# Kernel optimization log

Measured on AMD Instinct MI355X. Metric: run time of the kernel, lower is better.

The kernel has to match this reference:

```python
import jax, jax.numpy as jnp
import numpy as np

B, TQ, TK, N = 4, 128, 512, 1024   # batch, query len, key len, key_size
QS, VS, OS = 1024, 1024, 1024      # query_size, value_size, output_size


def setup_inputs() -> dict:
    key = jax.random.key(0)
    ks = jax.random.split(key, 9)
    s_q = 1.0 / np.sqrt(QS)
    s_k = 1.0 / np.sqrt(N)
    s_o = 1.0 / np.sqrt(QS + VS)
    return {
        "query": jax.random.normal(ks[0], (B, TQ, QS), jnp.float32),
        "keys": jax.random.normal(ks[1], (B, TK, N), jnp.float32),
        "values": jax.random.normal(ks[2], (B, TK, VS), jnp.float32),
        # linear_q: query_size -> key_size
        "Wq": jax.random.normal(ks[3], (N, QS), jnp.float32) * s_q,
        "bq": jax.random.normal(ks[4], (N,), jnp.float32) * s_q,
        # linear_att: key_size -> 1
        "w_att": jax.random.normal(ks[5], (N,), jnp.float32) * s_k,
        "b_att": jax.random.normal(ks[6], (), jnp.float32) * s_k,
        # linear_out: (query_size + value_size) -> output_size
        "Wout": jax.random.normal(ks[7], (OS, QS + VS), jnp.float32) * s_o,
        "bout": jax.random.normal(ks[8], (OS,), jnp.float32) * s_o,
    }


def reference(query, keys, values, Wq, bq, w_att, b_att, Wout, bout):
    # linear_q: [b, t_q, query_size] -> [b, t_q, n]
    att_query = jnp.einsum("bqe,ne->bqn", query, Wq) + bq
    # Bahdanau additive score: tanh(q + k) then linear_att (n -> 1)
    # intermediate is [b, t_q, t_k, n] as in the original module
    sum_qk = jnp.tanh(att_query[:, :, None, :] + keys[:, None, :, :])
    scores = jnp.einsum("bqkn,n->bqk", sum_qk, w_att) + b_att  # [b, t_q, t_k]
    scores_normalized = jax.nn.softmax(scores, axis=2)
    # context = softmax(scores) @ values  (dropout is identity with p=0)
    context = jnp.einsum("bqk,bkv->bqv", scores_normalized, values)
    # linear_out on concat([query, context]) + tanh
    cat = jnp.concatenate([query, context], axis=2)  # [b, t_q, q+v]
    out = jnp.tanh(jnp.einsum("bqc,oc->bqo", cat, Wout) + bout)
    return out, scores_normalized
```

## Files before the change

kernel.cpp:

```cpp
#include <hip/hip_runtime.h>
#include <math.h>

static constexpr int B_  = 4;
static constexpr int TQ  = 128;
static constexpr int TK  = 512;
static constexpr int NN  = 1024;
static constexpr int QS  = 1024;
static constexpr int VS  = 1024;
static constexpr int OS  = 1024;

#define K2F    2.8853900817779268f
#define LOG2EF 1.4426950408889634f
#define SLICE  524288

typedef __attribute__((ext_vector_type(8))) short bf16x8;
typedef __attribute__((ext_vector_type(4))) float f32x4;

#define MFMA16(a,b,c) __builtin_amdgcn_mfma_f32_16x16x32_bf16((a),(b),(c),0,0,0)

__device__ __forceinline__ ushort bf16_rne(float x) {
    uint u = __float_as_uint(x);
    u += 0x7FFFu + ((u >> 16) & 1u);
    return (ushort)(u >> 16);
}
__device__ __forceinline__ void split2(float x, ushort& h, ushort& l) {
    ushort hh = bf16_rne(x);
    float hv = __uint_as_float((uint)hh << 16);
    h = hh;
    l = bf16_rne(x - hv);
}

__global__ __launch_bounds__(256) void cvt_all_kernel(
    const float* __restrict__ Q, const float* __restrict__ Wq,
    const float* __restrict__ Wo, const float* __restrict__ V,
    ushort* __restrict__ Qh, ushort* __restrict__ Ql,
    ushort* __restrict__ Wqh, ushort* __restrict__ Wql,
    ushort* __restrict__ Woh,
    ushort* __restrict__ Vth)
{
    __shared__ float tile[64][65];
    const int bid = blockIdx.x;
    const int t = threadIdx.x;
    if (bid < 3584) {
        if (bid < 1536) {
            const float* src; ushort *h, *l; int idx;
            if (bid < 512) { src = Q;  h = Qh;  l = Ql;  idx = bid*256 + t; }
            else           { src = Wq; h = Wqh; l = Wql; idx = (bid-512)*256 + t; }
            float4 v = ((const float4*)src)[idx];
            ushort4 hh, ll;
            split2(v.x, hh.x, ll.x); split2(v.y, hh.y, ll.y);
            split2(v.z, hh.z, ll.z); split2(v.w, hh.w, ll.w);
            ((ushort4*)h)[idx] = hh;
            ((ushort4*)l)[idx] = ll;
        } else {
            int idx = (bid-1536)*256 + t;
            float4 v = ((const float4*)Wo)[idx];
            ushort4 hh;
            hh.x = bf16_rne(v.x); hh.y = bf16_rne(v.y);
            hh.z = bf16_rne(v.z); hh.w = bf16_rne(v.w);
            ((ushort4*)Woh)[idx] = hh;
        }
        return;
    }
    const int vid = bid - 3584;
    const int v0 = (vid & 15) * 64;
    const int k0 = ((vid >> 4) & 7) * 64;
    const int b  = vid >> 7;
    const float* src = V + ((size_t)b*TK + k0)*VS + v0;
    #pragma unroll
    for (int p = 0; p < 4; ++p) {
        int r = (t >> 4) + p*16, c = (t & 15) * 4;
        float4 vv = *(const float4*)(src + (size_t)r*VS + c);
        tile[r][c] = vv.x; tile[r][c+1] = vv.y; tile[r][c+2] = vv.z; tile[r][c+3] = vv.w;
    }
    __syncthreads();
    ushort* dh = Vth + (size_t)b*(VS*TK) + (size_t)v0*TK + k0;
    #pragma unroll
    for (int p = 0; p < 4; ++p) {
        int vr = (t >> 4) + p*16, kc = (t & 15) * 4;
        ushort4 hh;
        hh.x = bf16_rne(tile[kc+0][vr]);
        hh.y = bf16_rne(tile[kc+1][vr]);
        hh.z = bf16_rne(tile[kc+2][vr]);
        hh.w = bf16_rne(tile[kc+3][vr]);
        *(ushort4*)(dh + (size_t)vr*TK + kc) = hh;
    }
}

__global__ __launch_bounds__(256) void mfma_nt_kernel(
    const ushort* __restrict__ Ah, const ushort* __restrict__ Al,
    const ushort* __restrict__ Bh, const ushort* __restrict__ Bl,
    float* __restrict__ Cp, int lda, int ldb, int Nout, int kchunk, int bstride)
{
    __shared__ alignas(16) ushort lA[2][64][40];
    __shared__ alignas(16) ushort lB[2][64][40];
    const int t = threadIdx.x;
    const int m0 = blockIdx.y * 64, n0 = blockIdx.x * 64, kz = blockIdx.z;
    const int k0 = kz * kchunk;
    const int batch = m0 >> 7;
    const ushort* bhp = Bh + (size_t)batch * bstride;
    const ushort* blp = Bl + (size_t)batch * bstride;
    const int srow = t >> 2, skc = (t & 3) * 8;
    const int lane = t & 63, w = t >> 6;
    const int wm = (w >> 1) * 32, wn = (w & 1) * 32;
    const int fr = lane & 15, fg = (lane >> 4) * 8;

    f32x4 acc00 = {0,0,0,0}, acc01 = {0,0,0,0}, acc10 = {0,0,0,0}, acc11 = {0,0,0,0};

    for (int kb = k0; kb < k0 + kchunk; kb += 32) {
        uint4 va_h = *(const uint4*)(Ah  + (size_t)(m0+srow)*lda + kb + skc);
        uint4 va_l = *(const uint4*)(Al  + (size_t)(m0+srow)*lda + kb + skc);
        uint4 vb_h = *(const uint4*)(bhp + (size_t)(n0+srow)*ldb + kb + skc);
        uint4 vb_l = *(const uint4*)(blp + (size_t)(n0+srow)*ldb + kb + skc);
        *(uint4*)&lA[0][srow][skc] = va_h;
        *(uint4*)&lA[1][srow][skc] = va_l;
        *(uint4*)&lB[0][srow][skc] = vb_h;
        *(uint4*)&lB[1][srow][skc] = vb_l;
        __syncthreads();
        bf16x8 ah0 = *(const bf16x8*)&lA[0][wm + fr     ][fg];
        bf16x8 ah1 = *(const bf16x8*)&lA[0][wm + 16 + fr][fg];
        bf16x8 al0 = *(const bf16x8*)&lA[1][wm + fr     ][fg];
        bf16x8 al1 = *(const bf16x8*)&lA[1][wm + 16 + fr][fg];
        bf16x8 bh0 = *(const bf16x8*)&lB[0][wn + fr     ][fg];
        bf16x8 bh1 = *(const bf16x8*)&lB[0][wn + 16 + fr][fg];
        bf16x8 bl0 = *(const bf16x8*)&lB[1][wn + fr     ][fg];
        bf16x8 bl1 = *(const bf16x8*)&lB[1][wn + 16 + fr][fg];
        acc00 = MFMA16(ah0, bh0, acc00);
        acc00 = MFMA16(al0, bh0, acc00);
        acc00 = MFMA16(ah0, bl0, acc00);
        acc01 = MFMA16(ah0, bh1, acc01);
        acc01 = MFMA16(al0, bh1, acc01);
        acc01 = MFMA16(ah0, bl1, acc01);
        acc10 = MFMA16(ah1, bh0, acc10);
        acc10 = MFMA16(al1, bh0, acc10);
        acc10 = MFMA16(ah1, bl0, acc10);
        acc11 = MFMA16(ah1, bh1, acc11);
        acc11 = MFMA16(al1, bh1, acc11);
        acc11 = MFMA16(ah1, bl1, acc11);
        __syncthreads();
    }
    float* o = Cp + (size_t)kz * 512 * Nout;
    const int orow = (lane >> 4) * 4;
    #pragma unroll
    for (int r2 = 0; r2 < 4; ++r2) {
        o[(size_t)(m0+wm+orow+r2)*Nout      + n0+wn+fr]      = acc00[r2];
        o[(size_t)(m0+wm+orow+r2)*Nout      + n0+wn+16+fr]   = acc01[r2];
        o[(size_t)(m0+wm+16+orow+r2)*Nout   + n0+wn+fr]      = acc10[r2];
        o[(size_t)(m0+wm+16+orow+r2)*Nout   + n0+wn+16+fr]   = acc11[r2];
    }
}

__global__ __launch_bounds__(256) void mfma_nt2_kernel(
    const ushort* __restrict__ Ah, const ushort* __restrict__ Al,
    const ushort* __restrict__ Bh,
    float* __restrict__ Cp, int lda, int ldb, int Nout, int kchunk, int bstride)
{
    __shared__ alignas(16) ushort lA[2][64][40];
    __shared__ alignas(16) ushort lB[64][40];
    const int t = threadIdx.x;
    const int m0 = blockIdx.y * 64, n0 = blockIdx.x * 64, kz = blockIdx.z;
    const int k0 = kz * kchunk;
    const int batch = m0 >> 7;
    const ushort* bhp = Bh + (size_t)batch * bstride;
    const int srow = t >> 2, skc = (t & 3) * 8;
    const int lane = t & 63, w = t >> 6;
    const int wm = (w >> 1) * 32, wn = (w & 1) * 32;
    const int fr = lane & 15, fg = (lane >> 4) * 8;

    f32x4 acc00 = {0,0,0,0}, acc01 = {0,0,0,0}, acc10 = {0,0,0,0}, acc11 = {0,0,0,0};

    for (int kb = k0; kb < k0 + kchunk; kb += 32) {
        *(uint4*)&lA[0][srow][skc] = *(const uint4*)(Ah  + (size_t)(m0+srow)*lda + kb + skc);
        *(uint4*)&lA[1][srow][skc] = *(const uint4*)(Al  + (size_t)(m0+srow)*lda + kb + skc);
        *(uint4*)&lB[srow][skc]    = *(const uint4*)(bhp + (size_t)(n0+srow)*ldb + kb + skc);
        __syncthreads();
        bf16x8 ah0 = *(const bf16x8*)&lA[0][wm + fr     ][fg];
        bf16x8 ah1 = *(const bf16x8*)&lA[0][wm + 16 + fr][fg];
        bf16x8 al0 = *(const bf16x8*)&lA[1][wm + fr     ][fg];
        bf16x8 al1 = *(const bf16x8*)&lA[1][wm + 16 + fr][fg];
        bf16x8 bh0 = *(const bf16x8*)&lB[wn + fr     ][fg];
        bf16x8 bh1 = *(const bf16x8*)&lB[wn + 16 + fr][fg];
        acc00 = MFMA16(ah0, bh0, acc00);
        acc00 = MFMA16(al0, bh0, acc00);
        acc01 = MFMA16(ah0, bh1, acc01);
        acc01 = MFMA16(al0, bh1, acc01);
        acc10 = MFMA16(ah1, bh0, acc10);
        acc10 = MFMA16(al1, bh0, acc10);
        acc11 = MFMA16(ah1, bh1, acc11);
        acc11 = MFMA16(al1, bh1, acc11);
        __syncthreads();
    }
    float* o = Cp + (size_t)kz * 512 * Nout;
    const int orow = (lane >> 4) * 4;
    #pragma unroll
    for (int r2 = 0; r2 < 4; ++r2) {
        o[(size_t)(m0+wm+orow+r2)*Nout      + n0+wn+fr]      = acc00[r2];
        o[(size_t)(m0+wm+orow+r2)*Nout      + n0+wn+16+fr]   = acc01[r2];
        o[(size_t)(m0+wm+16+orow+r2)*Nout   + n0+wn+fr]      = acc10[r2];
        o[(size_t)(m0+wm+16+orow+r2)*Nout   + n0+wn+16+fr]   = acc11[r2];
    }
}

__global__ __launch_bounds__(256) void exp_combine_kernel(
    const float* __restrict__ Ap, const float* __restrict__ bias,
    float* __restrict__ E)
{
    int i = blockIdx.x * 256 + threadIdx.x;
    float4 p0 = ((const float4*)Ap)[i];
    float4 p1 = ((const float4*)(Ap + SLICE))[i];
    float4 p2 = ((const float4*)(Ap + 2*SLICE))[i];
    float4 p3 = ((const float4*)(Ap + 3*SLICE))[i];
    float4 bb = ((const float4*)bias)[i & 255];
    float4 r;
    r.x = exp2f((p0.x+p1.x+p2.x+p3.x+bb.x) * K2F);
    r.y = exp2f((p0.y+p1.y+p2.y+p3.y+bb.y) * K2F);
    r.z = exp2f((p0.z+p1.z+p2.z+p3.z+bb.z) * K2F);
    r.w = exp2f((p0.w+p1.w+p2.w+p3.w+bb.w) * K2F);
    ((float4*)E)[i] = r;
}

__global__ __launch_bounds__(256) void score_v8_kernel(
    const float* __restrict__ Ea,
    const float* __restrict__ keys,
    const float* __restrict__ watt,
    float* __restrict__ Sp)
{
    __shared__ float ea[64][66];
    __shared__ float ek[64][36];
    __shared__ float wl[64];
    const int tid = threadIdx.x;
    const int kt = blockIdx.x;
    const int qt = blockIdx.y;
    const int nh = blockIdx.z;
    const int q0 = qt * 64;
    const int b  = qt >> 1;
    const int k0 = b*TK + kt*32;
    const int tx = tid & 7;
    const int ty = tid >> 3;
    float acc[2][4] = {};

    #pragma unroll
    for (int half = 0; half < 2; ++half) {
        const int nbeg = nh*128 + half*64;
        if (half) __syncthreads();
        {
            const int q = tid >> 2;
            const int nc = (tid & 3) * 16;
            const float* ep = Ea + (size_t)(q0 + q)*NN + nbeg + nc;
            #pragma unroll
            for (int j4 = 0; j4 < 4; ++j4) {
                float4 ev = *(const float4*)(ep + j4*4);
                ea[nc+j4*4+0][q] = ev.x;
                ea[nc+j4*4+1][q] = ev.y;
                ea[nc+j4*4+2][q] = ev.z;
                ea[nc+j4*4+3][q] = ev.w;
            }
        }
        {
            const int k = tid >> 3;
            const int nc = (tid & 7) * 8;
            const float* kp = keys + (size_t)(k0 + k)*NN + nbeg + nc;
            #pragma unroll
            for (int j4 = 0; j4 < 2; ++j4) {
                float4 kv = *(const float4*)(kp + j4*4);
                ek[nc+j4*4+0][k] = exp2f(kv.x * K2F);
                ek[nc+j4*4+1][k] = exp2f(kv.y * K2F);
                ek[nc+j4*4+2][k] = exp2f(kv.z * K2F);
                ek[nc+j4*4+3][k] = exp2f(kv.w * K2F);
            }
        }
        if (tid < 64) wl[tid] = watt[nbeg + tid];
        __syncthreads();

        #pragma unroll 4
        for (int g = 0; g < 16; ++g) {
            float2 e0 = *(const float2*)&ea[4*g+0][ty*2];
            float2 e1 = *(const float2*)&ea[4*g+1][ty*2];
            float2 e2 = *(const float2*)&ea[4*g+2][ty*2];
            float2 e3 = *(const float2*)&ea[4*g+3][ty*2];
            float4 f0 = *(const float4*)&ek[4*g+0][tx*4];
            float4 f1 = *(const float4*)&ek[4*g+1][tx*4];
            float4 f2 = *(const float4*)&ek[4*g+2][tx*4];
            float4 f3 = *(const float4*)&ek[4*g+3][tx*4];
            float4 w4 = *(const float4*)&wl[4*g];
            float E0[2] = {e0.x, e0.y};
            float E1[2] = {e1.x, e1.y};
            float E2[2] = {e2.x, e2.y};
            float E3[2] = {e3.x, e3.y};
            float F0[4] = {f0.x, f0.y, f0.z, f0.w};
            float F1[4] = {f1.x, f1.y, f1.z, f1.w};
            float F2[4] = {f2.x, f2.y, f2.z, f2.w};
            float F3[4] = {f3.x, f3.y, f3.z, f3.w};
            #pragma unroll
            for (int i = 0; i < 2; ++i) {
                #pragma unroll
                for (int j = 0; j < 4; ++j) {
                    float A  = fmaf(E0[i], F0[j], 1.0f);
                    float Bv = fmaf(E1[i], F1[j], 1.0f);
                    float C  = fmaf(E2[i], F2[j], 1.0f);
                    float D  = fmaf(E3[i], F3[j], 1.0f);
                    float n0 = fmaf(w4.x, Bv, w4.y * A);
                    float n1 = fmaf(w4.z, D,  w4.w * C);
                    acc[i][j] = fmaf(n0, __builtin_amdgcn_rcpf(A * Bv), acc[i][j]);
                    acc[i][j] = fmaf(n1, __builtin_amdgcn_rcpf(C * D),  acc[i][j]);
                }
            }
        }
    }
    float* o = Sp + ((size_t)nh*512 + q0 + ty*2)*TK + kt*32 + tx*4;
    #pragma unroll
    for (int i = 0; i < 2; ++i) {
        float4 r = {-2.0f*acc[i][0], -2.0f*acc[i][1], -2.0f*acc[i][2], -2.0f*acc[i][3]};
        *(float4*)(o + (size_t)i*TK) = r;
    }
}

__global__ __launch_bounds__(256) void softmax_kernel(
    const float* __restrict__ Sp, float* __restrict__ P,
    ushort* __restrict__ Ph, ushort* __restrict__ Pl)
{
    const int lane = threadIdx.x & 63;
    const int wid  = threadIdx.x >> 6;
    const int row  = blockIdx.x * 4 + wid;
    const size_t S = (size_t)512*512;
    float v[8];
    float m = -3.4e38f;
    #pragma unroll
    for (int j = 0; j < 8; ++j) {
        int k = lane + j*64;
        float s = 0.f;
        #pragma unroll
        for (int h = 0; h < 8; ++h)
            s += Sp[h*S + (size_t)row*TK + k];
        v[j] = s;
        m = fmaxf(m, v[j]);
    }
    #pragma unroll
    for (int off = 32; off; off >>= 1) m = fmaxf(m, __shfl_xor(m, off, 64));
    float sum = 0.f;
    #pragma unroll
    for (int j = 0; j < 8; ++j) { v[j] = exp2f((v[j] - m) * LOG2EF); sum += v[j]; }
    #pragma unroll
    for (int off = 32; off; off >>= 1) sum += __shfl_xor(sum, off, 64);
    float inv = 1.0f / sum;
    #pragma unroll
    for (int j = 0; j < 8; ++j) {
        int k = lane + j*64;
        float pv = v[j] * inv;
        P[(size_t)row * TK + k] = pv;
        ushort h, l; split2(pv, h, l);
        Ph[(size_t)row * TK + k] = h;
        Pl[(size_t)row * TK + k] = l;
    }
}

__global__ __launch_bounds__(256) void combine_cvt_kernel(
    const float* __restrict__ Ep, ushort* __restrict__ Ch, ushort* __restrict__ Cl)
{
    int i = blockIdx.x * 256 + threadIdx.x;
    float4 p0 = ((const float4*)Ep)[i];
    float4 p1 = ((const float4*)(Ep + SLICE))[i];
    float4 p2 = ((const float4*)(Ep + 2*SLICE))[i];
    float4 p3 = ((const float4*)(Ep + 3*SLICE))[i];
    float4 s = {p0.x+p1.x+p2.x+p3.x, p0.y+p1.y+p2.y+p3.y,
                p0.z+p1.z+p2.z+p3.z, p0.w+p1.w+p2.w+p3.w};
    ushort4 hh, ll;
    split2(s.x, hh.x, ll.x); split2(s.y, hh.y, ll.y);
    split2(s.z, hh.z, ll.z); split2(s.w, hh.w, ll.w);
    ((ushort4*)Ch)[i] = hh;
    ((ushort4*)Cl)[i] = ll;
}

__global__ __launch_bounds__(256) void mfma_out_kernel(
    const ushort* __restrict__ Qh, const ushort* __restrict__ Ql,
    const ushort* __restrict__ Cxh, const ushort* __restrict__ Cxl,
    const ushort* __restrict__ Wh,
    float* __restrict__ Fp)
{
    __shared__ alignas(16) ushort lA[2][64][40];
    __shared__ alignas(16) ushort lB[64][40];
    const int t = threadIdx.x;
    const int m0 = blockIdx.y * 64, n0 = blockIdx.x * 64, kz = blockIdx.z;
    const ushort* ah_p = (kz < 2) ? Qh : Cxh;
    const ushort* al_p = (kz < 2) ? Ql : Cxl;
    const int akoff = (kz & 1) * 512;
    const int bkoff = kz * 512;
    const int srow = t >> 2, skc = (t & 3) * 8;
    const int lane = t & 63, w = t >> 6;
    const int wm = (w >> 1) * 32, wn = (w & 1) * 32;
    const int fr = lane & 15, fg = (lane >> 4) * 8;

    f32x4 acc00 = {0,0,0,0}, acc01 = {0,0,0,0}, acc10 = {0,0,0,0}, acc11 = {0,0,0,0};

    for (int kk = 0; kk < 512; kk += 32) {
        size_t aoff = (size_t)(m0+srow)*1024 + akoff + kk + skc;
        *(uint4*)&lA[0][srow][skc] = *(const uint4*)(ah_p + aoff);
        *(uint4*)&lA[1][srow][skc] = *(const uint4*)(al_p + aoff);
        *(uint4*)&lB[srow][skc] =
            *(const uint4*)(Wh + (size_t)(n0+srow)*2048 + bkoff + kk + skc);
        __syncthreads();
        bf16x8 ah0 = *(const bf16x8*)&lA[0][wm + fr     ][fg];
        bf16x8 ah1 = *(const bf16x8*)&lA[0][wm + 16 + fr][fg];
        bf16x8 al0 = *(const bf16x8*)&lA[1][wm + fr     ][fg];
        bf16x8 al1 = *(const bf16x8*)&lA[1][wm + 16 + fr][fg];
        bf16x8 bh0 = *(const bf16x8*)&lB[wn + fr     ][fg];
        bf16x8 bh1 = *(const bf16x8*)&lB[wn + 16 + fr][fg];
        acc00 = MFMA16(ah0, bh0, acc00);
        acc00 = MFMA16(al0, bh0, acc00);
        acc01 = MFMA16(ah0, bh1, acc01);
        acc01 = MFMA16(al0, bh1, acc01);
        acc10 = MFMA16(ah1, bh0, acc10);
        acc10 = MFMA16(al1, bh0, acc10);
        acc11 = MFMA16(ah1, bh1, acc11);
        acc11 = MFMA16(al1, bh1, acc11);
        __syncthreads();
    }
    float* o = Fp + (size_t)kz * SLICE;
    const int orow = (lane >> 4) * 4;
    #pragma unroll
    for (int r2 = 0; r2 < 4; ++r2) {
        o[(size_t)(m0+wm+orow+r2)*1024    + n0+wn+fr]    = acc00[r2];
        o[(size_t)(m0+wm+orow+r2)*1024    + n0+wn+16+fr] = acc01[r2];
        o[(size_t)(m0+wm+16+orow+r2)*1024 + n0+wn+fr]    = acc10[r2];
        o[(size_t)(m0+wm+16+orow+r2)*1024 + n0+wn+16+fr] = acc11[r2];
    }
}

__global__ __launch_bounds__(256) void tanh_combine_kernel(
    const float* __restrict__ Fp, const float* __restrict__ bias,
    float* __restrict__ out)
{
    int i = blockIdx.x * 256 + threadIdx.x;
    const size_t S = (size_t)B_*TQ*OS;
    float4 p0 = ((const float4*)Fp)[i];
    float4 p1 = ((const float4*)(Fp + S))[i];
    float4 p2 = ((const float4*)(Fp + 2*S))[i];
    float4 p3 = ((const float4*)(Fp + 3*S))[i];
    float4 bb = ((const float4*)bias)[i & 255];
    float4 r;
    r.x = tanhf(p0.x + p1.x + p2.x + p3.x + bb.x);
    r.y = tanhf(p0.y + p1.y + p2.y + p3.y + bb.y);
    r.z = tanhf(p0.z + p1.z + p2.z + p3.z + bb.z);
    r.w = tanhf(p0.w + p1.w + p2.w + p3.w + bb.w);
    ((float4*)out)[i] = r;
}

extern "C" void kernel_launch(void* const* d_in, const int* in_sizes, int n_in,
                              void* d_out, int out_size, void* d_ws, size_t ws_size,
                              hipStream_t stream)
{
    const float* query  = (const float*)d_in[0];
    const float* keys   = (const float*)d_in[1];
    const float* values = (const float*)d_in[2];
    const float* Wq     = (const float*)d_in[3];
    const float* bq     = (const float*)d_in[4];
    const float* watt   = (const float*)d_in[5];
    const float* Wout   = (const float*)d_in[7];
    const float* bout   = (const float*)d_in[8];

    float* out = (float*)d_out;
    float* P   = out + (size_t)B_*TQ*OS;

    char* base = (char*)d_ws;
    const size_t MB = 1u << 20;
    ushort* Qh  = (ushort*)(base +  0*MB);
    ushort* Ql  = (ushort*)(base +  1*MB);
    ushort* Wqh = (ushort*)(base +  2*MB);
    ushort* Wql = (ushort*)(base +  4*MB);
    ushort* Woh = (ushort*)(base +  6*MB);
    ushort* Vth = (ushort*)(base + 10*MB);
    float*  Ap  = (float*) (base + 14*MB);
    float*  Ea  = (float*) (base + 22*MB);
    float*  Sp  = (float*) (base + 24*MB);
    ushort* Ph  = (ushort*)(base + 32*MB);
    ushort* Pl  = (ushort*)(base + 32*MB + 512*1024);
    float*  Ep  = (float*) (base + 33*MB);
    ushort* Cxh = (ushort*)(base + 41*MB);
    ushort* Cxl = (ushort*)(base + 42*MB);
    float*  Fp  = (float*) (base + 43*MB);

    cvt_all_kernel<<<dim3(4096), dim3(256), 0, stream>>>(
        query, Wq, Wout, values, Qh, Ql, Wqh, Wql, Woh, Vth);
    mfma_nt_kernel<<<dim3(16, 8, 4), dim3(256), 0, stream>>>(
        Qh, Ql, Wqh, Wql, Ap, 1024, 1024, 1024, 256, 0);
    exp_combine_kernel<<<dim3(512), dim3(256), 0, stream>>>(Ap, bq, Ea);
    score_v8_kernel<<<dim3(16, 8, 8), dim3(256), 0, stream>>>(Ea, keys, watt, Sp);
    softmax_kernel<<<dim3(128), dim3(256), 0, stream>>>(Sp, P, Ph, Pl);
    mfma_nt2_kernel<<<dim3(16, 8, 4), dim3(256), 0, stream>>>(
        Ph, Pl, Vth, Ep, 512, 512, 1024, 128, VS*TK);
    combine_cvt_kernel<<<dim3(512), dim3(256), 0, stream>>>(Ep, Cxh, Cxl);
    mfma_out_kernel<<<dim3(16, 8, 4), dim3(256), 0, stream>>>(
        Qh, Ql, Cxh, Cxl, Woh, Fp);
    tanh_combine_kernel<<<dim3(512), dim3(256), 0, stream>>>(Fp, bout, out);
}
```

Baseline: 81.64 us.

## Retile score kernel to 512-thread blocks with 64 keys and 16-way n split

The additive-score kernel now uses 512-thread blocks covering 64 queries by 64 keys over a single 64-wide slice of the hidden dimension, replacing the two-pass loop over 128 n per block. The hidden dimension is split 16 ways instead of 8, so the softmax kernel now sums 16 partial score slices, and the workspace layout is shifted to make room for the larger partial buffer. The aim is more parallelism and fewer barriers per block, plus reuse of each exp(query) tile across twice as many keys. In exchange, the partial-score traffic written and re-read by softmax doubles.

```diff
diff --git a/kernel.cpp b/kernel.cpp
--- a/kernel.cpp
+++ b/kernel.cpp
@@ -219,95 +219,89 @@
     ((float4*)E)[i] = r;
 }
 
-__global__ __launch_bounds__(256) void score_v8_kernel(
+__global__ __launch_bounds__(512, 4) void score_v9_kernel(
     const float* __restrict__ Ea,
     const float* __restrict__ keys,
     const float* __restrict__ watt,
     float* __restrict__ Sp)
 {
     __shared__ float ea[64][66];
-    __shared__ float ek[64][36];
+    __shared__ float ek[64][68];
     __shared__ float wl[64];
     const int tid = threadIdx.x;
     const int kt = blockIdx.x;
     const int qt = blockIdx.y;
     const int nh = blockIdx.z;
+    const int nbeg = nh * 64;
     const int q0 = qt * 64;
     const int b  = qt >> 1;
-    const int k0 = b*TK + kt*32;
-    const int tx = tid & 7;
-    const int ty = tid >> 3;
+    const int k0 = b*TK + kt*64;
+
+    {
+        const int q = tid >> 3;
+        const int nc = (tid & 7) * 8;
+        const float* ep = Ea + (size_t)(q0 + q)*NN + nbeg + nc;
+        float4 e0 = *(const float4*)(ep);
+        float4 e1 = *(const float4*)(ep + 4);
+        ea[nc+0][q] = e0.x; ea[nc+1][q] = e0.y; ea[nc+2][q] = e0.z; ea[nc+3][q] = e0.w;
+        ea[nc+4][q] = e1.x; ea[nc+5][q] = e1.y; ea[nc+6][q] = e1.z; ea[nc+7][q] = e1.w;
+    }
+    {
+        const int k = tid >> 3;
+        const int nc = (tid & 7) * 8;
+        const float* kp = keys + (size_t)(k0 + k)*NN + nbeg + nc;
+        float4 k0v = *(const float4*)(kp);
+        float4 k1v = *(const float4*)(kp + 4);
+        ek[nc+0][k] = exp2f(k0v.x * K2F);
+        ek[nc+1][k] = exp2f(k0v.y * K2F);
+        ek[nc+2][k] = exp2f(k0v.z * K2F);
+        ek[nc+3][k] = exp2f(k0v.w * K2F);
+        ek[nc+4][k] = exp2f(k1v.x * K2F);
+        ek[nc+5][k] = exp2f(k1v.y * K2F);
+        ek[nc+6][k] = exp2f(k1v.z * K2F);
+        ek[nc+7][k] = exp2f(k1v.w * K2F);
+    }
+    if (tid < 64) wl[tid] = watt[nbeg + tid];
+    __syncthreads();
+
+    const int tx = tid & 15;
+    const int ty = tid >> 4;
     float acc[2][4] = {};
-
-    #pragma unroll
-    for (int half = 0; half < 2; ++half) {
-        const int nbeg = nh*128 + half*64;
-        if (half) __syncthreads();
-        {
-            const int q = tid >> 2;
-            const int nc = (tid & 3) * 16;
-            const float* ep = Ea + (size_t)(q0 + q)*NN + nbeg + nc;
+    #pragma unroll 4
+    for (int g = 0; g < 16; ++g) {
+        float2 e0 = *(const float2*)&ea[4*g+0][ty*2];
+        float2 e1 = *(const float2*)&ea[4*g+1][ty*2];
+        float2 e2 = *(const float2*)&ea[4*g+2][ty*2];
+        float2 e3 = *(const float2*)&ea[4*g+3][ty*2];
+        float4 f0 = *(const float4*)&ek[4*g+0][tx*4];
+        float4 f1 = *(const float4*)&ek[4*g+1][tx*4];
+        float4 f2 = *(const float4*)&ek[4*g+2][tx*4];
+        float4 f3 = *(const float4*)&ek[4*g+3][tx*4];
+        float4 w4 = *(const float4*)&wl[4*g];
+        float E0[2] = {e0.x, e0.y};
+        float E1[2] = {e1.x, e1.y};
+        float E2[2] = {e2.x, e2.y};
+        float E3[2] = {e3.x, e3.y};
+        float F0[4] = {f0.x, f0.y, f0.z, f0.w};
+        float F1[4] = {f1.x, f1.y, f1.z, f1.w};
+        float F2[4] = {f2.x, f2.y, f2.z, f2.w};
+        float F3[4] = {f3.x, f3.y, f3.z, f3.w};
+        #pragma unroll
+        for (int i = 0; i < 2; ++i) {
             #pragma unroll
-            for (int j4 = 0; j4 < 4; ++j4) {
-                float4 ev = *(const float4*)(ep + j4*4);
-                ea[nc+j4*4+0][q] = ev.x;
-                ea[nc+j4*4+1][q] = ev.y;
-                ea[nc+j4*4+2][q] = ev.z;
-                ea[nc+j4*4+3][q] = ev.w;
+            for (int j = 0; j < 4; ++j) {
+                float A  = fmaf(E0[i], F0[j], 1.0f);
+                float Bv = fmaf(E1[i], F1[j], 1.0f);
+                float C  = fmaf(E2[i], F2[j], 1.0f);
+                float D  = fmaf(E3[i], F3[j], 1.0f);
+                float n0 = fmaf(w4.x, Bv, w4.y * A);
+                float n1 = fmaf(w4.z, D,  w4.w * C);
+                acc[i][j] = fmaf(n0, __builtin_amdgcn_rcpf(A * Bv), acc[i][j]);
+                acc[i][j] = fmaf(n1, __builtin_amdgcn_rcpf(C * D),  acc[i][j]);
             }
         }
-        {
-            const int k = tid >> 3;
-            const int nc = (tid & 7) * 8;
-            const float* kp = keys + (size_t)(k0 + k)*NN + nbeg + nc;
-            #pragma unroll
-            for (int j4 = 0; j4 < 2; ++j4) {
-                float4 kv = *(const float4*)(kp + j4*4);
-                ek[nc+j4*4+0][k] = exp2f(kv.x * K2F);
-                ek[nc+j4*4+1][k] = exp2f(kv.y * K2F);
-                ek[nc+j4*4+2][k] = exp2f(kv.z * K2F);
-                ek[nc+j4*4+3][k] = exp2f(kv.w * K2F);
-            }
-        }
-        if (tid < 64) wl[tid] = watt[nbeg + tid];
-        __syncthreads();
-
-        #pragma unroll 4
-        for (int g = 0; g < 16; ++g) {
-            float2 e0 = *(const float2*)&ea[4*g+0][ty*2];
-            float2 e1 = *(const float2*)&ea[4*g+1][ty*2];
-            float2 e2 = *(const float2*)&ea[4*g+2][ty*2];
-            float2 e3 = *(const float2*)&ea[4*g+3][ty*2];
-            float4 f0 = *(const float4*)&ek[4*g+0][tx*4];
-            float4 f1 = *(const float4*)&ek[4*g+1][tx*4];
-            float4 f2 = *(const float4*)&ek[4*g+2][tx*4];
-            float4 f3 = *(const float4*)&ek[4*g+3][tx*4];
-            float4 w4 = *(const float4*)&wl[4*g];
-            float E0[2] = {e0.x, e0.y};
-            float E1[2] = {e1.x, e1.y};
-            float E2[2] = {e2.x, e2.y};
-            float E3[2] = {e3.x, e3.y};
-            float F0[4] = {f0.x, f0.y, f0.z, f0.w};
-            float F1[4] = {f1.x, f1.y, f1.z, f1.w};
-            float F2[4] = {f2.x, f2.y, f2.z, f2.w};
-            float F3[4] = {f3.x, f3.y, f3.z, f3.w};
-            #pragma unroll
-            for (int i = 0; i < 2; ++i) {
-                #pragma unroll
-                for (int j = 0; j < 4; ++j) {
-                    float A  = fmaf(E0[i], F0[j], 1.0f);
-                    float Bv = fmaf(E1[i], F1[j], 1.0f);
-                    float C  = fmaf(E2[i], F2[j], 1.0f);
-                    float D  = fmaf(E3[i], F3[j], 1.0f);
-                    float n0 = fmaf(w4.x, Bv, w4.y * A);
-                    float n1 = fmaf(w4.z, D,  w4.w * C);
-                    acc[i][j] = fmaf(n0, __builtin_amdgcn_rcpf(A * Bv), acc[i][j]);
-                    acc[i][j] = fmaf(n1, __builtin_amdgcn_rcpf(C * D),  acc[i][j]);
-                }
-            }
-        }
-    }
-    float* o = Sp + ((size_t)nh*512 + q0 + ty*2)*TK + kt*32 + tx*4;
+    }
+    float* o = Sp + ((size_t)nh*512 + q0 + ty*2)*TK + kt*64 + tx*4;
     #pragma unroll
     for (int i = 0; i < 2; ++i) {
         float4 r = {-2.0f*acc[i][0], -2.0f*acc[i][1], -2.0f*acc[i][2], -2.0f*acc[i][3]};
@@ -330,7 +324,7 @@
         int k = lane + j*64;
         float s = 0.f;
         #pragma unroll
-        for (int h = 0; h < 8; ++h)
+        for (int h = 0; h < 16; ++h)
             s += Sp[h*S + (size_t)row*TK + k];
         v[j] = s;
         m = fmaxf(m, v[j]);
@@ -472,19 +466,19 @@
     float*  Ap  = (float*) (base + 14*MB);
     float*  Ea  = (float*) (base + 22*MB);
     float*  Sp  = (float*) (base + 24*MB);
-    ushort* Ph  = (ushort*)(base + 32*MB);
-    ushort* Pl  = (ushort*)(base + 32*MB + 512*1024);
-    float*  Ep  = (float*) (base + 33*MB);
-    ushort* Cxh = (ushort*)(base + 41*MB);
-    ushort* Cxl = (ushort*)(base + 42*MB);
-    float*  Fp  = (float*) (base + 43*MB);
+    ushort* Ph  = (ushort*)(base + 40*MB);
+    ushort* Pl  = (ushort*)(base + 40*MB + 512*1024);
+    float*  Ep  = (float*) (base + 41*MB);
+    ushort* Cxh = (ushort*)(base + 49*MB);
+    ushort* Cxl = (ushort*)(base + 50*MB);
+    float*  Fp  = (float*) (base + 51*MB);
 
     cvt_all_kernel<<<dim3(4096), dim3(256), 0, stream>>>(
         query, Wq, Wout, values, Qh, Ql, Wqh, Wql, Woh, Vth);
     mfma_nt_kernel<<<dim3(16, 8, 4), dim3(256), 0, stream>>>(
         Qh, Ql, Wqh, Wql, Ap, 1024, 1024, 1024, 256, 0);
     exp_combine_kernel<<<dim3(512), dim3(256), 0, stream>>>(Ap, bq, Ea);
-    score_v8_kernel<<<dim3(16, 8, 8), dim3(256), 0, stream>>>(Ea, keys, watt, Sp);
+    score_v9_kernel<<<dim3(8, 8, 16), dim3(512), 0, stream>>>(Ea, keys, watt, Sp);
     softmax_kernel<<<dim3(128), dim3(256), 0, stream>>>(Sp, P, Ph, Pl);
     mfma_nt2_kernel<<<dim3(16, 8, 4), dim3(256), 0, stream>>>(
         Ph, Pl, Vth, Ep, 512, 512, 1024, 128, VS*TK);
```

Result: no change. 81.55 us (-0.1%).

## Enlarge score kernel register tile to 4x8 and split N into 16 slices

Applied to the files above, without the earlier changes.

The additive-score kernel now gives each thread a 4x8 output tile instead of 2x4 and covers 128 keys per block instead of 32. The N reduction is split into 16 slices of 64 rather than 8 slices of 128. This raises arithmetic per LDS load and reuses the exp(keys) tile across more queries, with launch bounds hinting at 2 blocks per CU. The trade-off is a doubled partial-score buffer (16 slices) that softmax must read and sum, more registers per thread, fewer blocks in flight, and shifted workspace offsets.

```diff
diff --git a/kernel.cpp b/kernel.cpp
--- a/kernel.cpp
+++ b/kernel.cpp
@@ -219,99 +219,101 @@
     ((float4*)E)[i] = r;
 }
 
-__global__ __launch_bounds__(256) void score_v8_kernel(
+__global__ __launch_bounds__(256, 2) void score_v10_kernel(
     const float* __restrict__ Ea,
     const float* __restrict__ keys,
     const float* __restrict__ watt,
     float* __restrict__ Sp)
 {
     __shared__ float ea[64][66];
-    __shared__ float ek[64][36];
+    __shared__ float ek[64][132];
     __shared__ float wl[64];
     const int tid = threadIdx.x;
     const int kt = blockIdx.x;
     const int qt = blockIdx.y;
     const int nh = blockIdx.z;
+    const int nbeg = nh * 64;
     const int q0 = qt * 64;
     const int b  = qt >> 1;
-    const int k0 = b*TK + kt*32;
-    const int tx = tid & 7;
-    const int ty = tid >> 3;
-    float acc[2][4] = {};
-
-    #pragma unroll
-    for (int half = 0; half < 2; ++half) {
-        const int nbeg = nh*128 + half*64;
-        if (half) __syncthreads();
-        {
-            const int q = tid >> 2;
-            const int nc = (tid & 3) * 16;
-            const float* ep = Ea + (size_t)(q0 + q)*NN + nbeg + nc;
+    const int k0 = b*TK + kt*128;
+
+    {
+        const int q = tid >> 2;
+        const int nc = (tid & 3) * 16;
+        const float* ep = Ea + (size_t)(q0 + q)*NN + nbeg + nc;
+        #pragma unroll
+        for (int j4 = 0; j4 < 4; ++j4) {
+            float4 ev = *(const float4*)(ep + j4*4);
+            ea[nc+j4*4+0][q] = ev.x;
+            ea[nc+j4*4+1][q] = ev.y;
+            ea[nc+j4*4+2][q] = ev.z;
+            ea[nc+j4*4+3][q] = ev.w;
+        }
+    }
+    {
+        const int k = tid >> 1;
+        const int nc = (tid & 1) * 32;
+        const float* kp = keys + (size_t)(k0 + k)*NN + nbeg + nc;
+        #pragma unroll
+        for (int j4 = 0; j4 < 8; ++j4) {
+            float4 kv = *(const float4*)(kp + j4*4);
+            ek[nc+j4*4+0][k] = exp2f(kv.x * K2F);
+            ek[nc+j4*4+1][k] = exp2f(kv.y * K2F);
+            ek[nc+j4*4+2][k] = exp2f(kv.z * K2F);
+            ek[nc+j4*4+3][k] = exp2f(kv.w * K2F);
+        }
+    }
+    if (tid < 64) wl[tid] = watt[nbeg + tid];
+    __syncthreads();
+
+    const int tx = tid & 15;
+    const int ty = tid >> 4;
+    float acc[4][8] = {};
+    #pragma unroll 2
+    for (int g = 0; g < 16; ++g) {
+        float4 e0 = *(const float4*)&ea[4*g+0][ty*4];
+        float4 e1 = *(const float4*)&ea[4*g+1][ty*4];
+        float4 e2 = *(const float4*)&ea[4*g+2][ty*4];
+        float4 e3 = *(const float4*)&ea[4*g+3][ty*4];
+        float4 f0a = *(const float4*)&ek[4*g+0][tx*8];
+        float4 f0b = *(const float4*)&ek[4*g+0][tx*8+4];
+        float4 f1a = *(const float4*)&ek[4*g+1][tx*8];
+        float4 f1b = *(const float4*)&ek[4*g+1][tx*8+4];
+        float4 f2a = *(const float4*)&ek[4*g+2][tx*8];
+        float4 f2b = *(const float4*)&ek[4*g+2][tx*8+4];
+        float4 f3a = *(const float4*)&ek[4*g+3][tx*8];
+        float4 f3b = *(const float4*)&ek[4*g+3][tx*8+4];
+        float4 w4 = *(const float4*)&wl[4*g];
+        float E0[4] = {e0.x,e0.y,e0.z,e0.w};
+        float E1[4] = {e1.x,e1.y,e1.z,e1.w};
+        float E2[4] = {e2.x,e2.y,e2.z,e2.w};
+        float E3[4] = {e3.x,e3.y,e3.z,e3.w};
+        float F0[8] = {f0a.x,f0a.y,f0a.z,f0a.w, f0b.x,f0b.y,f0b.z,f0b.w};
+        float F1[8] = {f1a.x,f1a.y,f1a.z,f1a.w, f1b.x,f1b.y,f1b.z,f1b.w};
+        float F2[8] = {f2a.x,f2a.y,f2a.z,f2a.w, f2b.x,f2b.y,f2b.z,f2b.w};
+        float F3[8] = {f3a.x,f3a.y,f3a.z,f3a.w, f3b.x,f3b.y,f3b.z,f3b.w};
+        #pragma unroll
+        for (int i = 0; i < 4; ++i) {
             #pragma unroll
-            for (int j4 = 0; j4 < 4; ++j4) {
-                float4 ev = *(const float4*)(ep + j4*4);
-                ea[nc+j4*4+0][q] = ev.x;
-                ea[nc+j4*4+1][q] = ev.y;
-                ea[nc+j4*4+2][q] = ev.z;
-                ea[nc+j4*4+3][q] = ev.w;
+            for (int j = 0; j < 8; ++j) {
+                float A  = fmaf(E0[i], F0[j], 1.0f);
+                float Bv = fmaf(E1[i], F1[j], 1.0f);
+                float C  = fmaf(E2[i], F2[j], 1.0f);
+                float D  = fmaf(E3[i], F3[j], 1.0f);
+                float n0 = fmaf(w4.x, Bv, w4.y * A);
+                float n1 = fmaf(w4.z, D,  w4.w * C);
+                acc[i][j] = fmaf(n0, __builtin_amdgcn_rcpf(A * Bv), acc[i][j]);
+                acc[i][j] = fmaf(n1, __builtin_amdgcn_rcpf(C * D),  acc[i][j]);
             }
         }
-        {
-            const int k = tid >> 3;
-            const int nc = (tid & 7) * 8;
-            const float* kp = keys + (size_t)(k0 + k)*NN + nbeg + nc;
-            #pragma unroll
-            for (int j4 = 0; j4 < 2; ++j4) {
-                float4 kv = *(const float4*)(kp + j4*4);
-                ek[nc+j4*4+0][k] = exp2f(kv.x * K2F);
-                ek[nc+j4*4+1][k] = exp2f(kv.y * K2F);
-                ek[nc+j4*4+2][k] = exp2f(kv.z * K2F);
-                ek[nc+j4*4+3][k] = exp2f(kv.w * K2F);
-            }
-        }
-        if (tid < 64) wl[tid] = watt[nbeg + tid];
-        __syncthreads();
-
-        #pragma unroll 4
-        for (int g = 0; g < 16; ++g) {
-            float2 e0 = *(const float2*)&ea[4*g+0][ty*2];
-            float2 e1 = *(const float2*)&ea[4*g+1][ty*2];
-            float2 e2 = *(const float2*)&ea[4*g+2][ty*2];
-            float2 e3 = *(const float2*)&ea[4*g+3][ty*2];
-            float4 f0 = *(const float4*)&ek[4*g+0][tx*4];
-            float4 f1 = *(const float4*)&ek[4*g+1][tx*4];
-            float4 f2 = *(const float4*)&ek[4*g+2][tx*4];
-            float4 f3 = *(const float4*)&ek[4*g+3][tx*4];
-            float4 w4 = *(const float4*)&wl[4*g];
-            float E0[2] = {e0.x, e0.y};
-            float E1[2] = {e1.x, e1.y};
-            float E2[2] = {e2.x, e2.y};
-            float E3[2] = {e3.x, e3.y};
-            float F0[4] = {f0.x, f0.y, f0.z, f0.w};
-            float F1[4] = {f1.x, f1.y, f1.z, f1.w};
-            float F2[4] = {f2.x, f2.y, f2.z, f2.w};
-            float F3[4] = {f3.x, f3.y, f3.z, f3.w};
-            #pragma unroll
-            for (int i = 0; i < 2; ++i) {
-                #pragma unroll
-                for (int j = 0; j < 4; ++j) {
-                    float A  = fmaf(E0[i], F0[j], 1.0f);
-                    float Bv = fmaf(E1[i], F1[j], 1.0f);
-                    float C  = fmaf(E2[i], F2[j], 1.0f);
-                    float D  = fmaf(E3[i], F3[j], 1.0f);
-                    float n0 = fmaf(w4.x, Bv, w4.y * A);
-                    float n1 = fmaf(w4.z, D,  w4.w * C);
-                    acc[i][j] = fmaf(n0, __builtin_amdgcn_rcpf(A * Bv), acc[i][j]);
-                    acc[i][j] = fmaf(n1, __builtin_amdgcn_rcpf(C * D),  acc[i][j]);
-                }
-            }
-        }
-    }
-    float* o = Sp + ((size_t)nh*512 + q0 + ty*2)*TK + kt*32 + tx*4;
-    #pragma unroll
-    for (int i = 0; i < 2; ++i) {
-        float4 r = {-2.0f*acc[i][0], -2.0f*acc[i][1], -2.0f*acc[i][2], -2.0f*acc[i][3]};
-        *(float4*)(o + (size_t)i*TK) = r;
+    }
+    float* o = Sp + ((size_t)nh*512 + q0 + ty*4)*TK + kt*128 + tx*8;
+    #pragma unroll
+    for (int i = 0; i < 4; ++i) {
+        float4 r0 = {-2.0f*acc[i][0], -2.0f*acc[i][1], -2.0f*acc[i][2], -2.0f*acc[i][3]};
+        float4 r1 = {-2.0f*acc[i][4], -2.0f*acc[i][5], -2.0f*acc[i][6], -2.0f*acc[i][7]};
+        *(float4*)(o + (size_t)i*TK)     = r0;
+        *(float4*)(o + (size_t)i*TK + 4) = r1;
     }
 }
 
@@ -330,7 +332,7 @@
         int k = lane + j*64;
         float s = 0.f;
         #pragma unroll
-        for (int h = 0; h < 8; ++h)
+        for (int h = 0; h < 16; ++h)
             s += Sp[h*S + (size_t)row*TK + k];
         v[j] = s;
         m = fmaxf(m, v[j]);
@@ -472,19 +474,19 @@
     float*  Ap  = (float*) (base + 14*MB);
     float*  Ea  = (float*) (base + 22*MB);
     float*  Sp  = (float*) (base + 24*MB);
-    ushort* Ph  = (ushort*)(base + 32*MB);
-    ushort* Pl  = (ushort*)(base + 32*MB + 512*1024);
-    float*  Ep  = (float*) (base + 33*MB);
-    ushort* Cxh = (ushort*)(base + 41*MB);
-    ushort* Cxl = (ushort*)(base + 42*MB);
-    float*  Fp  = (float*) (base + 43*MB);
+    ushort* Ph  = (ushort*)(base + 40*MB);
+    ushort* Pl  = (ushort*)(base + 40*MB + 512*1024);
+    float*  Ep  = (float*) (base + 41*MB);
+    ushort* Cxh = (ushort*)(base + 49*MB);
+    ushort* Cxl = (ushort*)(base + 50*MB);
+    float*  Fp  = (float*) (base + 51*MB);
 
     cvt_all_kernel<<<dim3(4096), dim3(256), 0, stream>>>(
         query, Wq, Wout, values, Qh, Ql, Wqh, Wql, Woh, Vth);
     mfma_nt_kernel<<<dim3(16, 8, 4), dim3(256), 0, stream>>>(
         Qh, Ql, Wqh, Wql, Ap, 1024, 1024, 1024, 256, 0);
     exp_combine_kernel<<<dim3(512), dim3(256), 0, stream>>>(Ap, bq, Ea);
-    score_v8_kernel<<<dim3(16, 8, 8), dim3(256), 0, stream>>>(Ea, keys, watt, Sp);
+    score_v10_kernel<<<dim3(4, 8, 16), dim3(256), 0, stream>>>(Ea, keys, watt, Sp);
     softmax_kernel<<<dim3(128), dim3(256), 0, stream>>>(Sp, P, Ph, Pl);
     mfma_nt2_kernel<<<dim3(16, 8, 4), dim3(256), 0, stream>>>(
         Ph, Pl, Vth, Ep, 512, 512, 1024, 128, VS*TK);
```

Result: slower. 86.13 us (+5.5%).
